# Kernel tuning notes

Measured on AMD Instinct MI355X. Metric: run time of the kernel, lower is better.

The kernel has to match this reference:

```python
import jax, jax.numpy as jnp
import numpy as np

B, N, D = 4, 4096, 256
H = 4
HD = D // H
FF = max(2 * D, 16)
EPS = 1e-5


def layer_norm(x, w, b):
    mu = jnp.mean(x, axis=-1, keepdims=True)
    var = jnp.mean(jnp.square(x - mu), axis=-1, keepdims=True)
    return (x - mu) * jax.lax.rsqrt(var + EPS) * w + b


def setup_inputs() -> dict:
    key = jax.random.key(0)
    ks = jax.random.split(key, 12)
    s = 1.0 / np.sqrt(D)
    sf = 1.0 / np.sqrt(FF)
    return {
        "tokens": jax.random.normal(ks[0], (B, N, D), jnp.float32),
        "importance": jax.random.normal(ks[1], (B, N), jnp.float32),
        "norm1_w": jnp.ones((D,), jnp.float32),
        "norm1_b": jnp.zeros((D,), jnp.float32),
        "Wq": jax.random.uniform(ks[2], (D, D), jnp.float32, -s, s),
        "bq": jnp.zeros((D,), jnp.float32),
        "Wk": jax.random.uniform(ks[3], (D, D), jnp.float32, -s, s),
        "bk": jnp.zeros((D,), jnp.float32),
        "Wv": jax.random.uniform(ks[4], (D, D), jnp.float32, -s, s),
        "bv": jnp.zeros((D,), jnp.float32),
        "Wo": jax.random.uniform(ks[5], (D, D), jnp.float32, -s, s),
        "bo": jnp.zeros((D,), jnp.float32),
        "norm2_w": jnp.ones((D,), jnp.float32),
        "norm2_b": jnp.zeros((D,), jnp.float32),
        "W1": jax.random.uniform(ks[6], (D, FF), jnp.float32, -s, s),
        "b1": jnp.zeros((FF,), jnp.float32),
        "W2": jax.random.uniform(ks[7], (FF, D), jnp.float32, -sf, sf),
        "b2": jnp.zeros((D,), jnp.float32),
    }


def reference(tokens, importance, norm1_w, norm1_b, Wq, bq, Wk, bk, Wv, bv,
              Wo, bo, norm2_w, norm2_b, W1, b1, W2, b2):
    # pre-norm MHA with additive importance bias
    x = layer_norm(tokens, norm1_w, norm1_b)
    q = (x @ Wq + bq).reshape(B, N, H, HD).transpose(0, 2, 1, 3)  # [B,H,N,HD]
    k = (x @ Wk + bk).reshape(B, N, H, HD).transpose(0, 2, 1, 3)
    v = (x @ Wv + bv).reshape(B, N, H, HD).transpose(0, 2, 1, 3)
    scores = jnp.einsum("bhnd,bhmd->bhnm", q, k) / np.sqrt(HD)
    scores = scores + importance[:, None, None, :]  # bias over key dim
    attn = jax.nn.softmax(scores, axis=-1)
    ctx = jnp.einsum("bhnm,bhmd->bhnd", attn, v)
    ctx = ctx.transpose(0, 2, 1, 3).reshape(B, N, D)
    x = tokens + (ctx @ Wo + bo)
    # GELU FFN (exact erf gelu, matching torch default)
    y = layer_norm(x, norm2_w, norm2_b)
    y = jax.nn.gelu(y @ W1 + b1, approximate=False) @ W2 + b2
    return x + y
```

## Files before the change

kernel.cpp:

```cpp
#include <hip/hip_runtime.h>

#define Bb 4
#define Nn 4096
#define Dd 256
#define Hh 4
#define HDd 64
#define FFf 512
#define MT 16384

typedef __attribute__((ext_vector_type(8))) short short8;
typedef __attribute__((ext_vector_type(4))) float f32x4;
typedef __attribute__((ext_vector_type(16))) float f32x16;
typedef unsigned short u16;
typedef unsigned int u32;
typedef __attribute__((ext_vector_type(4))) u32 u32x4;

typedef __attribute__((address_space(1))) const void glb_src;
typedef __attribute__((address_space(3))) void lds_dst;

__device__ __forceinline__ void gload_lds16(const void* g, void* l) {
    __builtin_amdgcn_global_load_lds((glb_src*)g, (lds_dst*)l, 16, 0, 0);
}

__device__ __forceinline__ u16 f2bf(float f) {
    union { float f; u32 i; } v; v.f = f;
    u32 r = v.i + 0x7FFFu + ((v.i >> 16) & 1u);
    return (u16)(r >> 16);
}

__device__ __forceinline__ short8 ld8(const u16* p) {
    return *(const short8*)p;
}

__device__ __forceinline__ void pl32swap(u32& a, u32& b) {
    asm("v_permlane32_swap_b32 %0, %1" : "+v"(a), "+v"(b));
}
__device__ __forceinline__ float xhalf_max(float x) {
    u32 a = __float_as_uint(x), b = a;
    pl32swap(a, b);
    return fmaxf(__uint_as_float(a), __uint_as_float(b));
}
__device__ __forceinline__ u32 cvtpk(float lo, float hi) {
    u32 r;
    asm("v_cvt_pk_bf16_f32 %0, %1, %2" : "=v"(r) : "v"(lo), "v"(hi));
    return r;
}
__device__ __forceinline__ float fexp2(float x) {
    float r;
    asm("v_exp_f32 %0, %1" : "=v"(r) : "v"(x));
    return r;
}
__device__ __forceinline__ float max3f(float a, float b, float c) {
    float r;
    asm("v_max3_f32 %0, %1, %2, %3" : "=v"(r) : "v"(a), "v"(b), "v"(c));
    return r;
}

#define QSCALE 0.18033610062f
#define LOG2E  1.44269504089f

__global__ __launch_bounds__(256) void prep_kernel(
        const float* __restrict__ Wq, const float* __restrict__ Wk,
        const float* __restrict__ Wv, const float* __restrict__ Wo,
        const float* __restrict__ W1, const float* __restrict__ W2,
        const float* __restrict__ imp,
        u16* __restrict__ WqkvT, u16* __restrict__ WoT,
        u16* __restrict__ W1T, u16* __restrict__ W2T,
        u32* __restrict__ impPk) {
    int e = blockIdx.x * 256 + threadIdx.x;
    if (e < 196608) {
        int c = e >> 8, k = e & 255;
        int mat = c >> 8;
        int cc = c & 255;
        const float* W = (mat == 0) ? Wq : ((mat == 1) ? Wk : Wv);
        WqkvT[(size_t)c * 256 + k] = f2bf(W[k * 256 + cc]);
    } else if (e < 262144) {
        int i = e - 196608; int n = i >> 8, k = i & 255;
        WoT[n * 256 + k] = f2bf(Wo[k * 256 + n]);
    } else if (e < 393216) {
        int i = e - 262144; int n = i >> 8, k = i & 255;
        W1T[n * 256 + k] = f2bf(W1[k * 512 + n]);
    } else if (e < 524288) {
        int i = e - 393216; int n = i >> 9, k = i & 511;
        W2T[n * 512 + k] = f2bf(W2[k * 256 + n]);
    } else {
        int i = e - 524288;
        float ivs = imp[i] * LOG2E;
        u16 ih = f2bf(ivs);
        float rem = ivs - __uint_as_float(((u32)ih) << 16);
        u16 il = f2bf(rem);
        impPk[i] = ((u32)il << 16) | ih;
    }
}

__global__ __launch_bounds__(256) void ln_kernel(const float* __restrict__ x,
        const float* __restrict__ w, const float* __restrict__ bia,
        u16* __restrict__ out) {
    int lane = threadIdx.x & 63;
    int row = blockIdx.x * 4 + (threadIdx.x >> 6);
    const float* xr = x + (size_t)row * Dd;
    float4 v = *(const float4*)(xr + lane * 4);
    float s = v.x + v.y + v.z + v.w;
    float s2 = v.x * v.x + v.y * v.y + v.z * v.z + v.w * v.w;
    #pragma unroll
    for (int off = 1; off < 64; off <<= 1) {
        s  += __shfl_xor(s, off);
        s2 += __shfl_xor(s2, off);
    }
    float mu = s * (1.0f / Dd);
    float var = s2 * (1.0f / Dd) - mu * mu;
    float rstd = rsqrtf(var + 1e-5f);
    float4 wv = *(const float4*)(w + lane * 4);
    float4 bv = *(const float4*)(bia + lane * 4);
    ushort4 ov;
    ov.x = f2bf((v.x - mu) * rstd * wv.x + bv.x);
    ov.y = f2bf((v.y - mu) * rstd * wv.y + bv.y);
    ov.z = f2bf((v.z - mu) * rstd * wv.z + bv.z);
    ov.w = f2bf((v.w - mu) * rstd * wv.w + bv.w);
    *(ushort4*)(out + (size_t)row * Dd + lane * 4) = ov;
}

template<int MODE, int KD, int BM>
__global__ __launch_bounds__(256) void gemm_bt(
        const u16* __restrict__ A, const u16* __restrict__ BT,
        const float* __restrict__ bias0, const float* __restrict__ bias1,
        const float* __restrict__ bias2,
        const float* __restrict__ resid, float* __restrict__ outf,
        u16* __restrict__ o0, u16* __restrict__ o1, u16* __restrict__ o2) {
    constexpr int AM = BM / 32;
    __shared__ u16 Asl[BM * 32];
    __shared__ u16 Bsl[128 * 32];
    int lane = threadIdx.x & 63;
    int wv = threadIdx.x >> 6;
    int wm = wv >> 1, wn = wv & 1;
    int m0 = blockIdx.y * BM, n0 = blockIdx.x * 128;
    f32x4 zz; zz[0] = 0.f; zz[1] = 0.f; zz[2] = 0.f; zz[3] = 0.f;
    f32x4 acc[AM][4];
    #pragma unroll
    for (int i = 0; i < AM; ++i)
        #pragma unroll
        for (int j = 0; j < 4; ++j) acc[i][j] = zz;

    for (int kt = 0; kt < KD; kt += 32) {
        __syncthreads();
        #pragma unroll
        for (int i = 0; i < BM / 64; ++i) {
            int chunk = threadIdx.x + i * 256;
            int row = chunk >> 2, c16 = chunk & 3;
            int srcc = (c16 ^ (row & 3)) * 8;
            gload_lds16(A + (size_t)(m0 + row) * KD + kt + srcc,
                        (char*)Asl + wv * 1024 + i * 4096);
        }
        #pragma unroll
        for (int i = 0; i < 2; ++i) {
            int chunk = threadIdx.x + i * 256;
            int row = chunk >> 2, c16 = chunk & 3;
            int srcc = (c16 ^ (row & 3)) * 8;
            gload_lds16(BT + (size_t)(n0 + row) * KD + kt + srcc,
                        (char*)Bsl + wv * 1024 + i * 4096);
        }
        __syncthreads();
        short8 af[AM], bfr[4];
        #pragma unroll
        for (int t = 0; t < AM; ++t) {
            int arow = wm * (BM / 2) + t * 16 + (lane & 15);
            af[t] = ld8(Asl + arow * 32 + (((lane >> 4) * 8) ^ ((arow & 3) * 8)));
        }
        #pragma unroll
        for (int t = 0; t < 4; ++t) {
            int brow = wn * 64 + t * 16 + (lane & 15);
            bfr[t] = ld8(Bsl + brow * 32 + (((lane >> 4) * 8) ^ ((brow & 3) * 8)));
        }
        #pragma unroll
        for (int mt = 0; mt < AM; ++mt)
            #pragma unroll
            for (int nt = 0; nt < 4; ++nt)
                acc[mt][nt] = __builtin_amdgcn_mfma_f32_16x16x32_bf16(af[mt], bfr[nt], acc[mt][nt], 0, 0, 0);
    }

    #pragma unroll
    for (int mt = 0; mt < AM; ++mt) {
        #pragma unroll
        for (int nt = 0; nt < 4; ++nt) {
            #pragma unroll
            for (int r = 0; r < 4; ++r) {
                int row = m0 + wm * (BM / 2) + mt * 16 + (lane >> 4) * 4 + r;
                int col = n0 + wn * 64 + nt * 16 + (lane & 15);
                float v = acc[mt][nt][r];
                if (MODE == 0) {
                    int mat = col >> 8;
                    int cc = col & 255;
                    int hh = cc >> 6, dd = cc & 63;
                    int bbi = row >> 12, nni = row & 4095;
                    int bh = bbi * Hh + hh;
                    if (mat == 0)      o0[((size_t)bh * Nn + nni) * HDd + dd] = f2bf((v + bias0[cc]) * QSCALE);
                    else if (mat == 1) o1[((size_t)bh * Nn + nni) * HDd + dd] = f2bf(v + bias1[cc]);
                    else               o2[((size_t)bh * HDd + dd) * Nn + nni] = f2bf(v + bias2[cc]);
                } else if (MODE == 2) {
                    float xg = v + bias0[col];
                    float g = 0.5f * xg * (1.0f + erff(xg * 0.70710678118654752f));
                    o0[(size_t)row * FFf + col] = f2bf(g);
                } else {
                    outf[(size_t)row * Dd + col] = resid[(size_t)row * Dd + col] + v + bias0[col];
                }
            }
        }
    }
}

__global__ __launch_bounds__(256) void oproj_ln_kernel(
        const u16* __restrict__ A, const u16* __restrict__ BT,
        const float* __restrict__ bias, const float* __restrict__ resid,
        const float* __restrict__ lnw, const float* __restrict__ lnb,
        float* __restrict__ x2, u16* __restrict__ yln) {
    __shared__ u16 Asl[32 * 32];
    __shared__ u16 Bsl[256 * 32];
    __shared__ float xlds[32][256];
    int lane = threadIdx.x & 63;
    int wv = threadIdx.x >> 6;
    int m0 = blockIdx.x * 32;
    f32x4 zz; zz[0] = 0.f; zz[1] = 0.f; zz[2] = 0.f; zz[3] = 0.f;
    f32x4 acc[2][4];
    #pragma unroll
    for (int i = 0; i < 2; ++i)
        #pragma unroll
        for (int j = 0; j < 4; ++j) acc[i][j] = zz;

    for (int kt = 0; kt < Dd; kt += 32) {
        __syncthreads();
        if (wv < 2) {
            int t = threadIdx.x;
            int row = t >> 2, c16 = t & 3;
            int srcc = (c16 ^ (row & 3)) * 8;
            gload_lds16(A + (size_t)(m0 + row) * Dd + kt + srcc,
                        (char*)Asl + wv * 1024);
        }
        #pragma unroll
        for (int i = 0; i < 4; ++i) {
            int chunk = threadIdx.x + i * 256;
            int row = chunk >> 2, c16 = chunk & 3;
            int srcc = (c16 ^ (row & 3)) * 8;
            gload_lds16(BT + (size_t)row * Dd + kt + srcc,
                        (char*)Bsl + wv * 1024 + i * 4096);
        }
        __syncthreads();
        short8 af[2], bfr[4];
        #pragma unroll
        for (int t = 0; t < 2; ++t) {
            int arow = t * 16 + (lane & 15);
            af[t] = ld8(Asl + arow * 32 + (((lane >> 4) * 8) ^ ((arow & 3) * 8)));
        }
        #pragma unroll
        for (int t = 0; t < 4; ++t) {
            int brow = wv * 64 + t * 16 + (lane & 15);
            bfr[t] = ld8(Bsl + brow * 32 + (((lane >> 4) * 8) ^ ((brow & 3) * 8)));
        }
        #pragma unroll
        for (int mt = 0; mt < 2; ++mt)
            #pragma unroll
            for (int nt = 0; nt < 4; ++nt)
                acc[mt][nt] = __builtin_amdgcn_mfma_f32_16x16x32_bf16(af[mt], bfr[nt], acc[mt][nt], 0, 0, 0);
    }

    #pragma unroll
    for (int mt = 0; mt < 2; ++mt) {
        #pragma unroll
        for (int nt = 0; nt < 4; ++nt) {
            #pragma unroll
            for (int r = 0; r < 4; ++r) {
                int row = mt * 16 + (lane >> 4) * 4 + r;
                int col = wv * 64 + nt * 16 + (lane & 15);
                float v = resid[(size_t)(m0 + row) * Dd + col] + acc[mt][nt][r] + bias[col];
                x2[(size_t)(m0 + row) * Dd + col] = v;
                xlds[row][col] = v;
            }
        }
    }
    __syncthreads();

    int rw = threadIdx.x >> 3;
    int cg = (threadIdx.x & 7) * 32;
    float s = 0.f, s2 = 0.f;
    #pragma unroll
    for (int j = 0; j < 32; ++j) {
        float v = xlds[rw][cg + j];
        s += v; s2 += v * v;
    }
    #pragma unroll
    for (int off = 1; off < 8; off <<= 1) {
        s  += __shfl_xor(s, off);
        s2 += __shfl_xor(s2, off);
    }
    float mu = s * (1.0f / Dd);
    float var = s2 * (1.0f / Dd) - mu * mu;
    float rstd = rsqrtf(var + 1e-5f);
    u16* op = yln + (size_t)(m0 + rw) * Dd + cg;
    #pragma unroll
    for (int j = 0; j < 32; j += 8) {
        float v0 = (xlds[rw][cg + j + 0] - mu) * rstd * lnw[cg + j + 0] + lnb[cg + j + 0];
        float v1 = (xlds[rw][cg + j + 1] - mu) * rstd * lnw[cg + j + 1] + lnb[cg + j + 1];
        float v2 = (xlds[rw][cg + j + 2] - mu) * rstd * lnw[cg + j + 2] + lnb[cg + j + 2];
        float v3 = (xlds[rw][cg + j + 3] - mu) * rstd * lnw[cg + j + 3] + lnb[cg + j + 3];
        float v4 = (xlds[rw][cg + j + 4] - mu) * rstd * lnw[cg + j + 4] + lnb[cg + j + 4];
        float v5 = (xlds[rw][cg + j + 5] - mu) * rstd * lnw[cg + j + 5] + lnb[cg + j + 5];
        float v6 = (xlds[rw][cg + j + 6] - mu) * rstd * lnw[cg + j + 6] + lnb[cg + j + 6];
        float v7 = (xlds[rw][cg + j + 7] - mu) * rstd * lnw[cg + j + 7] + lnb[cg + j + 7];
        uint4 pk;
        pk.x = cvtpk(v0, v1); pk.y = cvtpk(v2, v3);
        pk.z = cvtpk(v4, v5); pk.w = cvtpk(v6, v7);
        *(uint4*)(op + j) = pk;
    }
}

__global__ __launch_bounds__(256, 4) void attn_kernel(
        const u16* __restrict__ Qb, const u16* __restrict__ Kb,
        const u16* __restrict__ VTb, const u32* __restrict__ impPk,
        u16* __restrict__ pc, float* __restrict__ pm, float* __restrict__ pl) {
    __shared__ u16 Klds[2][64 * 64];
    __shared__ u16 Vlds[2][64 * 64];
    int lane = threadIdx.x & 63;
    int wv = threadIdx.x >> 6;
    int kvh = blockIdx.x >> 9;
    int bh = (blockIdx.x >> 5) & 15;
    int qt = blockIdx.x & 31;
    int bbi = bh >> 2;
    int qrow0 = qt * 128 + wv * 32;
    int q = lane & 31;
    int hf = lane >> 5;
    int key0 = kvh * 2048;
    int pg = kvh * 16 + bh;

    short8 qf[4];
    #pragma unroll
    for (int ks = 0; ks < 4; ++ks)
        qf[ks] = ld8(Qb + ((size_t)bh * Nn + qrow0 + q) * HDd + ks * 16 + hf * 8);

    short8 onef = (short8)0;
    if (hf == 0) { onef[0] = (short)0x3F80; onef[1] = (short)0x3F80; }
    short8 aone;
    #pragma unroll
    for (int j = 0; j < 8; ++j) aone[j] = (short)0x3F80;

    int sr = lane >> 3;
    int sc = lane & 7;
    int swz = (sc ^ sr) * 8;
    const u16* kp = Kb + ((size_t)bh * Nn + key0 + wv * 16 + sr) * HDd + swz;
    const u16* vp = VTb + ((size_t)bh * HDd + wv * 16 + sr) * Nn + key0 + swz;
    size_t ib = (size_t)bbi * Nn;

    gload_lds16(kp,           (char*)Klds[0] + wv * 2048);
    gload_lds16(kp + 8 * HDd, (char*)Klds[0] + wv * 2048 + 1024);
    gload_lds16(vp,           (char*)Vlds[0] + wv * 2048);
    gload_lds16(vp + 8 * Nn,  (char*)Vlds[0] + wv * 2048 + 1024);
    kp += 64 * HDd; vp += 64;
    u32 npk0 = impPk[ib + key0 + q], npk1 = impPk[ib + key0 + 32 + q];

    f32x16 ctx[2], lacc;
    #pragma unroll
    for (int r = 0; r < 16; ++r) { ctx[0][r] = 0.f; ctx[1][r] = 0.f; lacc[r] = 0.f; }
    float m = -__builtin_inff();

    int cur = 0;
    for (int t = 0; t < 32; ++t) {
        __syncthreads();
        u32 pk0 = npk0, pk1 = npk1;
        if (t < 31) {
            gload_lds16(kp,           (char*)Klds[cur ^ 1] + wv * 2048);
            gload_lds16(kp + 8 * HDd, (char*)Klds[cur ^ 1] + wv * 2048 + 1024);
            gload_lds16(vp,           (char*)Vlds[cur ^ 1] + wv * 2048);
            gload_lds16(vp + 8 * Nn,  (char*)Vlds[cur ^ 1] + wv * 2048 + 1024);
            kp += 64 * HDd; vp += 64;
            npk0 = impPk[ib + key0 + t * 64 + 64 + q];
            npk1 = impPk[ib + key0 + t * 64 + 96 + q];
        }
        const u16* Kc = Klds[cur];
        const u16* Vc = Vlds[cur];

        f32x16 s0, s1;
        #pragma unroll
        for (int r = 0; r < 16; ++r) { s0[r] = 0.f; s1[r] = 0.f; }
        __builtin_amdgcn_s_setprio(1);
        #pragma unroll
        for (int ks = 0; ks < 4; ++ks) {
            short8 kf0 = ld8(Kc + q * 64 + (((ks * 2 + hf) ^ (q & 7)) * 8));
            short8 kf1 = ld8(Kc + (32 + q) * 64 + (((ks * 2 + hf) ^ (q & 7)) * 8));
            s0 = __builtin_amdgcn_mfma_f32_32x32x16_bf16(kf0, qf[ks], s0, 0, 0, 0);
            s1 = __builtin_amdgcn_mfma_f32_32x32x16_bf16(kf1, qf[ks], s1, 0, 0, 0);
        }
        short8 af0 = (short8)0, af1 = (short8)0;
        if (hf == 0) {
            af0[0] = (short)(pk0 & 0xFFFFu); af0[1] = (short)(pk0 >> 16);
            af1[0] = (short)(pk1 & 0xFFFFu); af1[1] = (short)(pk1 >> 16);
        }
        s0 = __builtin_amdgcn_mfma_f32_32x32x16_bf16(af0, onef, s0, 0, 0, 0);
        s1 = __builtin_amdgcn_mfma_f32_32x32x16_bf16(af1, onef, s1, 0, 0, 0);
        __builtin_amdgcn_s_setprio(0);

        float a0 = max3f(s0[0], s0[1], s0[2]);
        float a1 = max3f(s0[3], s0[4], s0[5]);
        float a2 = max3f(s0[6], s0[7], s0[8]);
        float a3 = max3f(s0[9], s0[10], s0[11]);
        float a4 = max3f(s0[12], s0[13], s0[14]);
        float b0 = max3f(s1[0], s1[1], s1[2]);
        float b1 = max3f(s1[3], s1[4], s1[5]);
        float b2 = max3f(s1[6], s1[7], s1[8]);
        float b3 = max3f(s1[9], s1[10], s1[11]);
        float b4 = max3f(s1[12], s1[13], s1[14]);
        float c0 = max3f(a0, a1, a2);
        float c1 = max3f(a3, a4, s0[15]);
        float c2 = max3f(b0, b1, b2);
        float c3 = max3f(b3, b4, s1[15]);
        float tm = fmaxf(max3f(c0, c1, c2), c3);
        tm = xhalf_max(tm);
        bool nore = __all(tm <= m + 8.0f);
        if (!nore) {
            float nm = fmaxf(m, tm);
            float al = fexp2(m - nm);
            lacc[0] *= al;
            #pragma unroll
            for (int r = 0; r < 16; ++r) { ctx[0][r] *= al; ctx[1][r] *= al; }
            m = nm;
        }
        #pragma unroll
        for (int r = 0; r < 16; ++r) { s0[r] = fexp2(s0[r] - m); s1[r] = fexp2(s1[r] - m); }

        u32 w0[8], w1[8];
        #pragma unroll
        for (int j = 0; j < 8; ++j) {
            w0[j] = cvtpk(s0[2 * j], s0[2 * j + 1]);
            w1[j] = cvtpk(s1[2 * j], s1[2 * j + 1]);
        }
        pl32swap(w0[0], w0[2]); pl32swap(w0[1], w0[3]);
        pl32swap(w0[4], w0[6]); pl32swap(w0[5], w0[7]);
        pl32swap(w1[0], w1[2]); pl32swap(w1[1], w1[3]);
        pl32swap(w1[4], w1[6]); pl32swap(w1[5], w1[7]);
        u32x4 t00; t00[0] = w0[0]; t00[1] = w0[1]; t00[2] = w0[2]; t00[3] = w0[3];
        u32x4 t01; t01[0] = w0[4]; t01[1] = w0[5]; t01[2] = w0[6]; t01[3] = w0[7];
        u32x4 t10; t10[0] = w1[0]; t10[1] = w1[1]; t10[2] = w1[2]; t10[3] = w1[3];
        u32x4 t11; t11[0] = w1[4]; t11[1] = w1[5]; t11[2] = w1[6]; t11[3] = w1[7];
        short8 pf00 = __builtin_bit_cast(short8, t00);
        short8 pf01 = __builtin_bit_cast(short8, t01);
        short8 pf10 = __builtin_bit_cast(short8, t10);
        short8 pf11 = __builtin_bit_cast(short8, t11);

        __builtin_amdgcn_s_setprio(1);
        lacc = __builtin_amdgcn_mfma_f32_32x32x16_bf16(aone, pf00, lacc, 0, 0, 0);
        lacc = __builtin_amdgcn_mfma_f32_32x32x16_bf16(aone, pf01, lacc, 0, 0, 0);
        lacc = __builtin_amdgcn_mfma_f32_32x32x16_bf16(aone, pf10, lacc, 0, 0, 0);
        lacc = __builtin_amdgcn_mfma_f32_32x32x16_bf16(aone, pf11, lacc, 0, 0, 0);
        #pragma unroll
        for (int dt = 0; dt < 2; ++dt) {
            int vrow = dt * 32 + q;
            const u16* vb = Vc + vrow * 64;
            int sw = vrow & 7;
            short8 vf;
            vf = ld8(vb + (((0 + hf) ^ sw) * 8));
            ctx[dt] = __builtin_amdgcn_mfma_f32_32x32x16_bf16(vf, pf00, ctx[dt], 0, 0, 0);
            vf = ld8(vb + (((2 + hf) ^ sw) * 8));
            ctx[dt] = __builtin_amdgcn_mfma_f32_32x32x16_bf16(vf, pf01, ctx[dt], 0, 0, 0);
            vf = ld8(vb + (((4 + hf) ^ sw) * 8));
            ctx[dt] = __builtin_amdgcn_mfma_f32_32x32x16_bf16(vf, pf10, ctx[dt], 0, 0, 0);
            vf = ld8(vb + (((6 + hf) ^ sw) * 8));
            ctx[dt] = __builtin_amdgcn_mfma_f32_32x32x16_bf16(vf, pf11, ctx[dt], 0, 0, 0);
        }
        __builtin_amdgcn_s_setprio(0);
        cur ^= 1;
    }

    int qg = qrow0 + q;
    if (hf == 0) {
        pm[(size_t)pg * Nn + qg] = m;
        pl[(size_t)pg * Nn + qg] = lacc[0];
    }
    #pragma unroll
    for (int dt = 0; dt < 2; ++dt) {
        #pragma unroll
        for (int r = 0; r < 16; ++r) {
            int d = dt * 32 + (r & 3) + 8 * (r >> 2) + 4 * hf;
            pc[((size_t)pg * 64 + d) * Nn + qg] = f2bf(ctx[dt][r]);
        }
    }
}

__global__ __launch_bounds__(256) void merge_kernel(
        const u16* __restrict__ pc, const float* __restrict__ pm,
        const float* __restrict__ pl, u16* __restrict__ ctxOut) {
    __shared__ float trans[64][65];
    __shared__ float f0a[64], f1a[64];
    int bh = blockIdx.x >> 6;
    int q0 = (blockIdx.x & 63) * 64;
    int t = threadIdx.x;
    if (t < 64) {
        int qg = q0 + t;
        float m0 = pm[(size_t)bh * Nn + qg];
        float m1 = pm[(size_t)(16 + bh) * Nn + qg];
        float l0 = pl[(size_t)bh * Nn + qg];
        float l1 = pl[(size_t)(16 + bh) * Nn + qg];
        float M = fmaxf(m0, m1);
        float w0 = fexp2(m0 - M), w1 = fexp2(m1 - M);
        float inv = 1.0f / (l0 * w0 + l1 * w1);
        f0a[t] = w0 * inv; f1a[t] = w1 * inv;
    }
    __syncthreads();
    int wv = t >> 6, lane = t & 63;
    #pragma unroll
    for (int i = 0; i < 16; ++i) {
        int d = wv * 16 + i;
        float c0 = __uint_as_float((u32)pc[((size_t)bh * 64 + d) * Nn + q0 + lane] << 16);
        float c1 = __uint_as_float((u32)pc[((size_t)(16 + bh) * 64 + d) * Nn + q0 + lane] << 16);
        trans[lane][d] = c0 * f0a[lane] + c1 * f1a[lane];
    }
    __syncthreads();
    int q = t >> 2, dg = t & 3;
    int b = bh >> 2, h = bh & 3;
    const float* tr = &trans[q][dg * 16];
    uint4 pa, pb;
    pa.x = cvtpk(tr[0], tr[1]);  pa.y = cvtpk(tr[2], tr[3]);
    pa.z = cvtpk(tr[4], tr[5]);  pa.w = cvtpk(tr[6], tr[7]);
    pb.x = cvtpk(tr[8], tr[9]);  pb.y = cvtpk(tr[10], tr[11]);
    pb.z = cvtpk(tr[12], tr[13]); pb.w = cvtpk(tr[14], tr[15]);
    u16* op = ctxOut + ((size_t)b * Nn + q0 + q) * Dd + h * 64 + dg * 16;
    *(uint4*)op = pa;
    *(uint4*)(op + 8) = pb;
}

extern "C" void kernel_launch(void* const* d_in, const int* in_sizes, int n_in,
                              void* d_out, int out_size, void* d_ws, size_t ws_size,
                              hipStream_t stream) {
    (void)in_sizes; (void)n_in; (void)out_size; (void)ws_size;
    const float* tokens     = (const float*)d_in[0];
    const float* importance = (const float*)d_in[1];
    const float* n1w = (const float*)d_in[2];
    const float* n1b = (const float*)d_in[3];
    const float* Wq  = (const float*)d_in[4];
    const float* bq  = (const float*)d_in[5];
    const float* Wk  = (const float*)d_in[6];
    const float* bk  = (const float*)d_in[7];
    const float* Wv  = (const float*)d_in[8];
    const float* bv  = (const float*)d_in[9];
    const float* Wo  = (const float*)d_in[10];
    const float* bo  = (const float*)d_in[11];
    const float* n2w = (const float*)d_in[12];
    const float* n2b = (const float*)d_in[13];
    const float* W1  = (const float*)d_in[14];
    const float* b1  = (const float*)d_in[15];
    const float* W2  = (const float*)d_in[16];
    const float* b2  = (const float*)d_in[17];
    float* out = (float*)d_out;

    char* ws = (char*)d_ws;
    const size_t MB = (size_t)1 << 20;
    u16* xln   = (u16*)(ws);
    u16* qb    = (u16*)(ws + 8 * MB);
    u16* kb    = (u16*)(ws + 16 * MB);
    u16* vT    = (u16*)(ws + 24 * MB);
    u16* ctx   = (u16*)(ws + 32 * MB);
    u16* pc    = (u16*)(ws + 40 * MB);
    float* pm  = (float*)(ws + 56 * MB);
    float* pl  = (float*)(ws + 56 * MB + 524288);
    u16* WqkvT = (u16*)(ws + 57 * MB);
    u16* WoT   = (u16*)(ws + 57 * MB + 393216);
    u16* W1T   = (u16*)(ws + 57 * MB + 393216 + 131072);
    u16* W2T   = (u16*)(ws + 57 * MB + 393216 + 131072 + 262144);
    u32* impPk = (u32*)(ws + 57 * MB + 393216 + 131072 + 262144 + 262144);
    u16* yln   = xln;
    u16* hbuf  = qb;
    float* x2  = out;

    prep_kernel<<<2112, 256, 0, stream>>>(Wq, Wk, Wv, Wo, W1, W2, importance,
                                          WqkvT, WoT, W1T, W2T, impPk);
    ln_kernel<<<4096, 256, 0, stream>>>(tokens, n1w, n1b, xln);
    gemm_bt<0, 256, 128><<<dim3(6, 128), 256, 0, stream>>>(xln, WqkvT, bq, bk, bv,
                                                           nullptr, nullptr, qb, kb, vT);
    attn_kernel<<<1024, 256, 0, stream>>>(qb, kb, vT, impPk, pc, pm, pl);
    merge_kernel<<<1024, 256, 0, stream>>>(pc, pm, pl, ctx);
    oproj_ln_kernel<<<512, 256, 0, stream>>>(ctx, WoT, bo, tokens, n2w, n2b, x2, yln);
    gemm_bt<2, 256, 64><<<dim3(4, 256), 256, 0, stream>>>(yln, W1T, b1, nullptr, nullptr,
                                                          nullptr, nullptr, hbuf, nullptr, nullptr);
    gemm_bt<3, 512, 64><<<dim3(2, 256), 256, 0, stream>>>(hbuf, W2T, b2, nullptr, nullptr,
                                                          x2, out, nullptr, nullptr, nullptr);
}
```

Baseline: 197.0 us.

## Process 64 query rows per wave in attention to reuse K/V fragments

Each wave in the attention kernel now handles two 32-row query groups instead of one, so every K and V fragment read from LDS feeds two MFMAs. The block count is halved (256 query rows per block) and launch bounds drop to 2 blocks per CU to allow the larger register footprint. The row-sum accumulator is shared between the two groups using split ones-vectors, and each group keeps its own running max. The aim is fewer LDS reads and K/V tile loads per unit of compute, at the cost of lower occupancy and fewer blocks (512) to fill the GPU.

```diff
diff --git a/kernel.cpp b/kernel.cpp
--- a/kernel.cpp
+++ b/kernel.cpp
@@ -312,7 +312,7 @@
     }
 }
 
-__global__ __launch_bounds__(256, 4) void attn_kernel(
+__global__ __launch_bounds__(256, 2) void attn_kernel(
         const u16* __restrict__ Qb, const u16* __restrict__ Kb,
         const u16* __restrict__ VTb, const u32* __restrict__ impPk,
         u16* __restrict__ pc, float* __restrict__ pm, float* __restrict__ pl) {
@@ -320,26 +320,33 @@
     __shared__ u16 Vlds[2][64 * 64];
     int lane = threadIdx.x & 63;
     int wv = threadIdx.x >> 6;
-    int kvh = blockIdx.x >> 9;
-    int bh = (blockIdx.x >> 5) & 15;
-    int qt = blockIdx.x & 31;
+    int kvh = blockIdx.x >> 8;
+    int bh = (blockIdx.x >> 4) & 15;
+    int qt = blockIdx.x & 15;
     int bbi = bh >> 2;
-    int qrow0 = qt * 128 + wv * 32;
+    int qrow0 = qt * 256 + wv * 64;
     int q = lane & 31;
     int hf = lane >> 5;
     int key0 = kvh * 2048;
     int pg = kvh * 16 + bh;
 
-    short8 qf[4];
-    #pragma unroll
-    for (int ks = 0; ks < 4; ++ks)
-        qf[ks] = ld8(Qb + ((size_t)bh * Nn + qrow0 + q) * HDd + ks * 16 + hf * 8);
+    short8 qfA[4], qfB[4];
+    #pragma unroll
+    for (int ks = 0; ks < 4; ++ks) {
+        qfA[ks] = ld8(Qb + ((size_t)bh * Nn + qrow0 + q) * HDd + ks * 16 + hf * 8);
+        qfB[ks] = ld8(Qb + ((size_t)bh * Nn + qrow0 + 32 + q) * HDd + ks * 16 + hf * 8);
+    }
 
     short8 onef = (short8)0;
     if (hf == 0) { onef[0] = (short)0x3F80; onef[1] = (short)0x3F80; }
-    short8 aone;
-    #pragma unroll
-    for (int j = 0; j < 8; ++j) aone[j] = (short)0x3F80;
+    short8 aoneLo = (short8)0, aoneHi = (short8)0;
+    if ((lane & 31) < 16) {
+        #pragma unroll
+        for (int j = 0; j < 8; ++j) aoneLo[j] = (short)0x3F80;
+    } else {
+        #pragma unroll
+        for (int j = 0; j < 8; ++j) aoneHi[j] = (short)0x3F80;
+    }
 
     int sr = lane >> 3;
     int sc = lane & 7;
@@ -355,10 +362,14 @@
     kp += 64 * HDd; vp += 64;
     u32 npk0 = impPk[ib + key0 + q], npk1 = impPk[ib + key0 + 32 + q];
 
-    f32x16 ctx[2], lacc;
-    #pragma unroll
-    for (int r = 0; r < 16; ++r) { ctx[0][r] = 0.f; ctx[1][r] = 0.f; lacc[r] = 0.f; }
-    float m = -__builtin_inff();
+    f32x16 ctxA[2], ctxB[2], lacc;
+    #pragma unroll
+    for (int r = 0; r < 16; ++r) {
+        ctxA[0][r] = 0.f; ctxA[1][r] = 0.f;
+        ctxB[0][r] = 0.f; ctxB[1][r] = 0.f;
+        lacc[r] = 0.f;
+    }
+    float mA = -__builtin_inff(), mB = -__builtin_inff();
 
     int cur = 0;
     for (int t = 0; t < 32; ++t) {
@@ -376,108 +387,161 @@
         const u16* Kc = Klds[cur];
         const u16* Vc = Vlds[cur];
 
-        f32x16 s0, s1;
-        #pragma unroll
-        for (int r = 0; r < 16; ++r) { s0[r] = 0.f; s1[r] = 0.f; }
+        f32x16 sA0, sA1, sB0, sB1;
+        #pragma unroll
+        for (int r = 0; r < 16; ++r) { sA0[r] = 0.f; sA1[r] = 0.f; sB0[r] = 0.f; sB1[r] = 0.f; }
         __builtin_amdgcn_s_setprio(1);
         #pragma unroll
         for (int ks = 0; ks < 4; ++ks) {
             short8 kf0 = ld8(Kc + q * 64 + (((ks * 2 + hf) ^ (q & 7)) * 8));
             short8 kf1 = ld8(Kc + (32 + q) * 64 + (((ks * 2 + hf) ^ (q & 7)) * 8));
-            s0 = __builtin_amdgcn_mfma_f32_32x32x16_bf16(kf0, qf[ks], s0, 0, 0, 0);
-            s1 = __builtin_amdgcn_mfma_f32_32x32x16_bf16(kf1, qf[ks], s1, 0, 0, 0);
+            sA0 = __builtin_amdgcn_mfma_f32_32x32x16_bf16(kf0, qfA[ks], sA0, 0, 0, 0);
+            sA1 = __builtin_amdgcn_mfma_f32_32x32x16_bf16(kf1, qfA[ks], sA1, 0, 0, 0);
+            sB0 = __builtin_amdgcn_mfma_f32_32x32x16_bf16(kf0, qfB[ks], sB0, 0, 0, 0);
+            sB1 = __builtin_amdgcn_mfma_f32_32x32x16_bf16(kf1, qfB[ks], sB1, 0, 0, 0);
         }
         short8 af0 = (short8)0, af1 = (short8)0;
         if (hf == 0) {
             af0[0] = (short)(pk0 & 0xFFFFu); af0[1] = (short)(pk0 >> 16);
             af1[0] = (short)(pk1 & 0xFFFFu); af1[1] = (short)(pk1 >> 16);
         }
-        s0 = __builtin_amdgcn_mfma_f32_32x32x16_bf16(af0, onef, s0, 0, 0, 0);
-        s1 = __builtin_amdgcn_mfma_f32_32x32x16_bf16(af1, onef, s1, 0, 0, 0);
+        sA0 = __builtin_amdgcn_mfma_f32_32x32x16_bf16(af0, onef, sA0, 0, 0, 0);
+        sA1 = __builtin_amdgcn_mfma_f32_32x32x16_bf16(af1, onef, sA1, 0, 0, 0);
+        sB0 = __builtin_amdgcn_mfma_f32_32x32x16_bf16(af0, onef, sB0, 0, 0, 0);
+        sB1 = __builtin_amdgcn_mfma_f32_32x32x16_bf16(af1, onef, sB1, 0, 0, 0);
         __builtin_amdgcn_s_setprio(0);
 
-        float a0 = max3f(s0[0], s0[1], s0[2]);
-        float a1 = max3f(s0[3], s0[4], s0[5]);
-        float a2 = max3f(s0[6], s0[7], s0[8]);
-        float a3 = max3f(s0[9], s0[10], s0[11]);
-        float a4 = max3f(s0[12], s0[13], s0[14]);
-        float b0 = max3f(s1[0], s1[1], s1[2]);
-        float b1 = max3f(s1[3], s1[4], s1[5]);
-        float b2 = max3f(s1[6], s1[7], s1[8]);
-        float b3 = max3f(s1[9], s1[10], s1[11]);
-        float b4 = max3f(s1[12], s1[13], s1[14]);
-        float c0 = max3f(a0, a1, a2);
-        float c1 = max3f(a3, a4, s0[15]);
-        float c2 = max3f(b0, b1, b2);
-        float c3 = max3f(b3, b4, s1[15]);
-        float tm = fmaxf(max3f(c0, c1, c2), c3);
-        tm = xhalf_max(tm);
-        bool nore = __all(tm <= m + 8.0f);
-        if (!nore) {
-            float nm = fmaxf(m, tm);
-            float al = fexp2(m - nm);
-            lacc[0] *= al;
+        {
+            float a0 = max3f(sA0[0], sA0[1], sA0[2]);
+            float a1 = max3f(sA0[3], sA0[4], sA0[5]);
+            float a2 = max3f(sA0[6], sA0[7], sA0[8]);
+            float a3 = max3f(sA0[9], sA0[10], sA0[11]);
+            float a4 = max3f(sA0[12], sA0[13], sA0[14]);
+            float b0 = max3f(sA1[0], sA1[1], sA1[2]);
+            float b1 = max3f(sA1[3], sA1[4], sA1[5]);
+            float b2 = max3f(sA1[6], sA1[7], sA1[8]);
+            float b3 = max3f(sA1[9], sA1[10], sA1[11]);
+            float b4 = max3f(sA1[12], sA1[13], sA1[14]);
+            float c0 = max3f(a0, a1, a2);
+            float c1 = max3f(a3, a4, sA0[15]);
+            float c2 = max3f(b0, b1, b2);
+            float c3 = max3f(b3, b4, sA1[15]);
+            float tm = xhalf_max(fmaxf(max3f(c0, c1, c2), c3));
+            bool nore = __all(tm <= mA + 8.0f);
+            if (!nore) {
+                float nm = fmaxf(mA, tm);
+                float al = fexp2(mA - nm);
+                #pragma unroll
+                for (int r = 0; r < 8; ++r) lacc[r] *= al;
+                #pragma unroll
+                for (int r = 0; r < 16; ++r) { ctxA[0][r] *= al; ctxA[1][r] *= al; }
+                mA = nm;
+            }
             #pragma unroll
-            for (int r = 0; r < 16; ++r) { ctx[0][r] *= al; ctx[1][r] *= al; }
-            m = nm;
-        }
-        #pragma unroll
-        for (int r = 0; r < 16; ++r) { s0[r] = fexp2(s0[r] - m); s1[r] = fexp2(s1[r] - m); }
-
-        u32 w0[8], w1[8];
+            for (int r = 0; r < 16; ++r) { sA0[r] = fexp2(sA0[r] - mA); sA1[r] = fexp2(sA1[r] - mA); }
+        }
+        {
+            float a0 = max3f(sB0[0], sB0[1], sB0[2]);
+            float a1 = max3f(sB0[3], sB0[4], sB0[5]);
+            float a2 = max3f(sB0[6], sB0[7], sB0[8]);
+            float a3 = max3f(sB0[9], sB0[10], sB0[11]);
+            float a4 = max3f(sB0[12], sB0[13], sB0[14]);
+            float b0 = max3f(sB1[0], sB1[1], sB1[2]);
+            float b1 = max3f(sB1[3], sB1[4], sB1[5]);
+            float b2 = max3f(sB1[6], sB1[7], sB1[8]);
+            float b3 = max3f(sB1[9], sB1[10], sB1[11]);
+            float b4 = max3f(sB1[12], sB1[13], sB1[14]);
+            float c0 = max3f(a0, a1, a2);
+            float c1 = max3f(a3, a4, sB0[15]);
+            float c2 = max3f(b0, b1, b2);
+            float c3 = max3f(b3, b4, sB1[15]);
+            float tm = xhalf_max(fmaxf(max3f(c0, c1, c2), c3));
+            bool nore = __all(tm <= mB + 8.0f);
+            if (!nore) {
+                float nm = fmaxf(mB, tm);
+                float al = fexp2(mB - nm);
+                #pragma unroll
+                for (int r = 8; r < 16; ++r) lacc[r] *= al;
+                #pragma unroll
+                for (int r = 0; r < 16; ++r) { ctxB[0][r] *= al; ctxB[1][r] *= al; }
+                mB = nm;
+            }
+            #pragma unroll
+            for (int r = 0; r < 16; ++r) { sB0[r] = fexp2(sB0[r] - mB); sB1[r] = fexp2(sB1[r] - mB); }
+        }
+
+        u32 wA0[8], wA1[8], wB0[8], wB1[8];
         #pragma unroll
         for (int j = 0; j < 8; ++j) {
-            w0[j] = cvtpk(s0[2 * j], s0[2 * j + 1]);
-            w1[j] = cvtpk(s1[2 * j], s1[2 * j + 1]);
-        }
-        pl32swap(w0[0], w0[2]); pl32swap(w0[1], w0[3]);
-        pl32swap(w0[4], w0[6]); pl32swap(w0[5], w0[7]);
-        pl32swap(w1[0], w1[2]); pl32swap(w1[1], w1[3]);
-        pl32swap(w1[4], w1[6]); pl32swap(w1[5], w1[7]);
-        u32x4 t00; t00[0] = w0[0]; t00[1] = w0[1]; t00[2] = w0[2]; t00[3] = w0[3];
-        u32x4 t01; t01[0] = w0[4]; t01[1] = w0[5]; t01[2] = w0[6]; t01[3] = w0[7];
-        u32x4 t10; t10[0] = w1[0]; t10[1] = w1[1]; t10[2] = w1[2]; t10[3] = w1[3];
-        u32x4 t11; t11[0] = w1[4]; t11[1] = w1[5]; t11[2] = w1[6]; t11[3] = w1[7];
-        short8 pf00 = __builtin_bit_cast(short8, t00);
-        short8 pf01 = __builtin_bit_cast(short8, t01);
-        short8 pf10 = __builtin_bit_cast(short8, t10);
-        short8 pf11 = __builtin_bit_cast(short8, t11);
+            wA0[j] = cvtpk(sA0[2 * j], sA0[2 * j + 1]);
+            wA1[j] = cvtpk(sA1[2 * j], sA1[2 * j + 1]);
+            wB0[j] = cvtpk(sB0[2 * j], sB0[2 * j + 1]);
+            wB1[j] = cvtpk(sB1[2 * j], sB1[2 * j + 1]);
+        }
+        pl32swap(wA0[0], wA0[2]); pl32swap(wA0[1], wA0[3]);
+        pl32swap(wA0[4], wA0[6]); pl32swap(wA0[5], wA0[7]);
+        pl32swap(wA1[0], wA1[2]); pl32swap(wA1[1], wA1[3]);
+        pl32swap(wA1[4], wA1[6]); pl32swap(wA1[5], wA1[7]);
+        pl32swap(wB0[0], wB0[2]); pl32swap(wB0[1], wB0[3]);
+        pl32swap(wB0[4], wB0[6]); pl32swap(wB0[5], wB0[7]);
+        pl32swap(wB1[0], wB1[2]); pl32swap(wB1[1], wB1[3]);
+        pl32swap(wB1[4], wB1[6]); pl32swap(wB1[5], wB1[7]);
+        short8 pfA[4], pfB[4];
+        {
+            u32x4 t0; t0[0] = wA0[0]; t0[1] = wA0[1]; t0[2] = wA0[2]; t0[3] = wA0[3];
+            u32x4 t1; t1[0] = wA0[4]; t1[1] = wA0[5]; t1[2] = wA0[6]; t1[3] = wA0[7];
+            u32x4 t2; t2[0] = wA1[0]; t2[1] = wA1[1]; t2[2] = wA1[2]; t2[3] = wA1[3];
+            u32x4 t3; t3[0] = wA1[4]; t3[1] = wA1[5]; t3[2] = wA1[6]; t3[3] = wA1[7];
+            pfA[0] = __builtin_bit_cast(short8, t0);
+            pfA[1] = __builtin_bit_cast(short8, t1);
+            pfA[2] = __builtin_bit_cast(short8, t2);
+            pfA[3] = __builtin_bit_cast(short8, t3);
+            u32x4 u0; u0[0] = wB0[0]; u0[1] = wB0[1]; u0[2] = wB0[2]; u0[3] = wB0[3];
+            u32x4 u1; u1[0] = wB0[4]; u1[1] = wB0[5]; u1[2] = wB0[6]; u1[3] = wB0[7];
+            u32x4 u2; u2[0] = wB1[0]; u2[1] = wB1[1]; u2[2] = wB1[2]; u2[3] = wB1[3];
+            u32x4 u3; u3[0] = wB1[4]; u3[1] = wB1[5]; u3[2] = wB1[6]; u3[3] = wB1[7];
+            pfB[0] = __builtin_bit_cast(short8, u0);
+            pfB[1] = __builtin_bit_cast(short8, u1);
+            pfB[2] = __builtin_bit_cast(short8, u2);
+            pfB[3] = __builtin_bit_cast(short8, u3);
+        }
 
         __builtin_amdgcn_s_setprio(1);
-        lacc = __builtin_amdgcn_mfma_f32_32x32x16_bf16(aone, pf00, lacc, 0, 0, 0);
-        lacc = __builtin_amdgcn_mfma_f32_32x32x16_bf16(aone, pf01, lacc, 0, 0, 0);
-        lacc = __builtin_amdgcn_mfma_f32_32x32x16_bf16(aone, pf10, lacc, 0, 0, 0);
-        lacc = __builtin_amdgcn_mfma_f32_32x32x16_bf16(aone, pf11, lacc, 0, 0, 0);
+        #pragma unroll
+        for (int j = 0; j < 4; ++j) {
+            lacc = __builtin_amdgcn_mfma_f32_32x32x16_bf16(aoneLo, pfA[j], lacc, 0, 0, 0);
+            lacc = __builtin_amdgcn_mfma_f32_32x32x16_bf16(aoneHi, pfB[j], lacc, 0, 0, 0);
+        }
         #pragma unroll
         for (int dt = 0; dt < 2; ++dt) {
             int vrow = dt * 32 + q;
             const u16* vb = Vc + vrow * 64;
             int sw = vrow & 7;
-            short8 vf;
-            vf = ld8(vb + (((0 + hf) ^ sw) * 8));
-            ctx[dt] = __builtin_amdgcn_mfma_f32_32x32x16_bf16(vf, pf00, ctx[dt], 0, 0, 0);
-            vf = ld8(vb + (((2 + hf) ^ sw) * 8));
-            ctx[dt] = __builtin_amdgcn_mfma_f32_32x32x16_bf16(vf, pf01, ctx[dt], 0, 0, 0);
-            vf = ld8(vb + (((4 + hf) ^ sw) * 8));
-            ctx[dt] = __builtin_amdgcn_mfma_f32_32x32x16_bf16(vf, pf10, ctx[dt], 0, 0, 0);
-            vf = ld8(vb + (((6 + hf) ^ sw) * 8));
-            ctx[dt] = __builtin_amdgcn_mfma_f32_32x32x16_bf16(vf, pf11, ctx[dt], 0, 0, 0);
+            #pragma unroll
+            for (int j = 0; j < 4; ++j) {
+                short8 vf = ld8(vb + (((2 * j + hf) ^ sw) * 8));
+                ctxA[dt] = __builtin_amdgcn_mfma_f32_32x32x16_bf16(vf, pfA[j], ctxA[dt], 0, 0, 0);
+                ctxB[dt] = __builtin_amdgcn_mfma_f32_32x32x16_bf16(vf, pfB[j], ctxB[dt], 0, 0, 0);
+            }
         }
         __builtin_amdgcn_s_setprio(0);
         cur ^= 1;
     }
 
-    int qg = qrow0 + q;
+    int qgA = qrow0 + q, qgB = qrow0 + 32 + q;
     if (hf == 0) {
-        pm[(size_t)pg * Nn + qg] = m;
-        pl[(size_t)pg * Nn + qg] = lacc[0];
+        pm[(size_t)pg * Nn + qgA] = mA;
+        pl[(size_t)pg * Nn + qgA] = lacc[0];
+        pm[(size_t)pg * Nn + qgB] = mB;
+        pl[(size_t)pg * Nn + qgB] = lacc[8];
     }
     #pragma unroll
     for (int dt = 0; dt < 2; ++dt) {
         #pragma unroll
         for (int r = 0; r < 16; ++r) {
             int d = dt * 32 + (r & 3) + 8 * (r >> 2) + 4 * hf;
-            pc[((size_t)pg * 64 + d) * Nn + qg] = f2bf(ctx[dt][r]);
+            pc[((size_t)pg * 64 + d) * Nn + qgA] = f2bf(ctxA[dt][r]);
+            pc[((size_t)pg * 64 + d) * Nn + qgB] = f2bf(ctxB[dt][r]);
         }
     }
 }
@@ -572,7 +636,7 @@
     ln_kernel<<<4096, 256, 0, stream>>>(tokens, n1w, n1b, xln);
     gemm_bt<0, 256, 128><<<dim3(6, 128), 256, 0, stream>>>(xln, WqkvT, bq, bk, bv,
                                                            nullptr, nullptr, qb, kb, vT);
-    attn_kernel<<<1024, 256, 0, stream>>>(qb, kb, vT, impPk, pc, pm, pl);
+    attn_kernel<<<512, 256, 0, stream>>>(qb, kb, vT, impPk, pc, pm, pl);
     merge_kernel<<<1024, 256, 0, stream>>>(pc, pm, pl, ctx);
     oproj_ln_kernel<<<512, 256, 0, stream>>>(ctx, WoT, bo, tokens, n2w, n2b, x2, yln);
     gemm_bt<2, 256, 64><<<dim3(4, 256), 256, 0, stream>>>(yln, W1T, b1, nullptr, nullptr,
```

Result: faster. 183.1 us (median of 2 runs) (-7.1%).
